# Kernel optimization log

Hardware: AMD Instinct MI355X
Metric: run time of the kernel (lower is better)

The kernel has to match this reference:

```python
import jax, jax.numpy as jnp
import numpy as np

B, NUM_RX, NUM_CHIRPS, SAMPLES = 16, 4, 64, 256
D_BINS, R_BINS = 64, 256


def _conv3d(x, w, b, pad):
    y = jax.lax.conv_general_dilated(x, w, (1, 1, 1), pad,
                                     dimension_numbers=('NCDHW', 'OIDHW', 'NCDHW'))
    return y + b[None, :, None, None, None]


def _conv2d(x, w, b, pad):
    y = jax.lax.conv_general_dilated(x, w, (1, 1), pad,
                                     dimension_numbers=('NCHW', 'OIHW', 'NCHW'))
    return y + b[None, :, None, None]


def _bn2(x, s, t):
    return x * s[None, :, None, None] + t[None, :, None, None]


def _bn3(x, s, t):
    return x * s[None, :, None, None, None] + t[None, :, None, None, None]


def _upsample_bilinear_ac(x, oh, ow):
    # torch Upsample(mode='bilinear', align_corners=True)
    _, _, h, w = x.shape
    ph = jnp.linspace(0.0, h - 1.0, oh)
    pw = jnp.linspace(0.0, w - 1.0, ow)
    h0 = jnp.clip(jnp.floor(ph).astype(jnp.int32), 0, h - 1)
    h1 = jnp.clip(h0 + 1, 0, h - 1)
    fh = ph - h0
    w0 = jnp.clip(jnp.floor(pw).astype(jnp.int32), 0, w - 1)
    w1 = jnp.clip(w0 + 1, 0, w - 1)
    fw = pw - w0
    x = x[:, :, h0, :] * (1.0 - fh)[None, None, :, None] + x[:, :, h1, :] * fh[None, None, :, None]
    x = x[:, :, :, w0] * (1.0 - fw) + x[:, :, :, w1] * fw
    return x


def setup_inputs() -> dict:
    ks = iter(jax.random.split(jax.random.key(0), 80))

    def nrm(shape, s=0.05):
        return s * jax.random.normal(next(ks), shape, dtype=jnp.float32)

    inp = {'x': jax.random.normal(next(ks), (B, NUM_RX, NUM_CHIRPS, SAMPLES, 2), dtype=jnp.float32)}

    def conv(name, shape):
        inp[name + '_w'] = nrm(shape)
        inp[name + '_b'] = nrm((shape[0],))

    def bn(name, n):  # BatchNorm in inference form folded to scale/shift
        inp[name + '_s'] = 1.0 + nrm((n,), 0.1)
        inp[name + '_t'] = nrm((n,), 0.1)

    conv('tc1', (16, 2, 1, 1, 3)); bn('tc1', 16)
    conv('tc2', (32, 16, 1, 1, 3)); bn('tc2', 32)
    conv('rx', (32, 32, NUM_RX, 1, 1)); bn('rx', 32)
    conv('cc1', (64, 32 * NUM_CHIRPS, 3, 3)); bn('cc1', 64)
    conv('cc2', (64, 64, 3, 3)); bn('cc2', 64)
    conv('rd1', (128, 64, 3, 3)); bn('rd1', 128)
    conv('rd2', (128, 128, 3, 3)); bn('rd2', 128)
    conv('up1', (64, 128, 3, 3)); bn('up1', 64)
    conv('up2', (32, 64, 3, 3)); bn('up2', 32)
    conv('up3', (1, 32, 1, 1))
    inp['wr'] = jax.random.normal(next(ks), (SAMPLES, R_BINS, 2), dtype=jnp.float32)
    inp['wd'] = jax.random.normal(next(ks), (NUM_CHIRPS, D_BINS, 2), dtype=jnp.float32)
    return inp


def reference(x, tc1_w, tc1_b, tc1_s, tc1_t, tc2_w, tc2_b, tc2_s, tc2_t,
              rx_w, rx_b, rx_s, rx_t, cc1_w, cc1_b, cc1_s, cc1_t,
              cc2_w, cc2_b, cc2_s, cc2_t, rd1_w, rd1_b, rd1_s, rd1_t,
              rd2_w, rd2_b, rd2_s, rd2_t, up1_w, up1_b, up1_s, up1_t,
              up2_w, up2_b, up2_s, up2_t, up3_w, up3_b, wr, wd):
    r = jax.nn.relu
    p3 = [(0, 0), (0, 0), (1, 1)]
    p2 = [(1, 1), (1, 1)]
    h = jnp.transpose(x, (0, 4, 1, 2, 3))                      # [B,2,RX,C,S]
    h = r(_bn3(_conv3d(h, tc1_w, tc1_b, p3), tc1_s, tc1_t))
    h = r(_bn3(_conv3d(h, tc2_w, tc2_b, p3), tc2_s, tc2_t))
    h = r(_bn3(_conv3d(h, rx_w, rx_b, [(0, 0)] * 3), rx_s, rx_t))[:, :, 0]  # [B,32,C,S]
    h = h.reshape(h.shape[0], -1, SAMPLES)[:, :, None, :]      # [B,32*C,1,S]
    h = r(_bn2(_conv2d(h, cc1_w, cc1_b, p2), cc1_s, cc1_t))
    h = r(_bn2(_conv2d(h, cc2_w, cc2_b, p2), cc2_s, cc2_t))
    h = r(_bn2(_conv2d(h, rd1_w, rd1_b, p2), rd1_s, rd1_t))
    h = r(_bn2(_conv2d(h, rd2_w, rd2_b, p2), rd2_s, rd2_t))
    h = _upsample_bilinear_ac(h, D_BINS, R_BINS)               # [B,128,D,R]
    h = r(_bn2(_conv2d(h, up1_w, up1_b, p2), up1_s, up1_t))
    h = r(_bn2(_conv2d(h, up2_w, up2_b, p2), up2_s, up2_t))
    h = jax.nn.sigmoid(_conv2d(h, up3_w, up3_b, [(0, 0), (0, 0)]))  # [B,1,D,R]
    # learnable_fft (input is real: x_imag = 0), loops -> two batched matmuls
    xr = h[:, 0]                                               # [B,D,R]
    rr = jnp.einsum('bcs,sr->bcr', xr, wr[:, :, 0])            # range DFT, real
    ri = jnp.einsum('bcs,sr->bcr', xr, wr[:, :, 1])            # range DFT, imag
    rdr = jnp.einsum('bcr,cd->bdr', rr, wd[:, :, 0]) - jnp.einsum('bcr,cd->bdr', ri, wd[:, :, 1])
    rdi = jnp.einsum('bcr,cd->bdr', rr, wd[:, :, 1]) + jnp.einsum('bcr,cd->bdr', ri, wd[:, :, 0])
    mag = jnp.sqrt(rdr * rdr + rdi * rdi) / (NUM_CHIRPS * SAMPLES)
    out = jnp.clip(h + 0.1 * mag[:, None], 0.0, 1.0)
    return jnp.transpose(out, (0, 2, 3, 1))                    # [B,D,R,1]
```

## Files before the change

kernel.cpp:

```cpp
#include <hip/hip_runtime.h>
#include <math.h>

#define OFF_A      0u
#define OFF_P      8388608u
#define OFF_WCC1   10485760u
#define OFF_BCC1   10878976u
#define OFF_WCC2   10879040u
#define OFF_BCC2   10895424u
#define OFF_WRD1   10895488u
#define OFF_BRD1   10928256u
#define OFF_WRD2   10928384u
#define OFF_BRD2   10993920u
#define OFF_WUP1   10994048u
#define OFF_BUP1   11092352u
#define OFF_WUP2   11092416u
#define OFF_BUP2   11215296u
#define OFF_WRX    11215328u
#define OFF_W1F    11219424u
#define OFF_B1F    11219520u
#define OFF_W2F    11219536u
#define OFF_B2F    11221072u
#define OFF_BRXF   11221104u
#define OFF_R      0u
#define OFF_H      524288u

__device__ __forceinline__ void fma4(float4& a, const float4& x, float w) {
  a.x = fmaf(x.x, w, a.x); a.y = fmaf(x.y, w, a.y);
  a.z = fmaf(x.z, w, a.z); a.w = fmaf(x.w, w, a.w);
}

__global__ __launch_bounds__(256) void k_repack(
    const float* __restrict__ tc1_w, const float* __restrict__ tc1_b, const float* __restrict__ tc1_s, const float* __restrict__ tc1_t,
    const float* __restrict__ tc2_w, const float* __restrict__ tc2_b, const float* __restrict__ tc2_s, const float* __restrict__ tc2_t,
    const float* __restrict__ rx_w, const float* __restrict__ rx_b, const float* __restrict__ rx_s, const float* __restrict__ rx_t,
    const float* __restrict__ cc1_w, const float* __restrict__ cc1_b, const float* __restrict__ cc1_s, const float* __restrict__ cc1_t,
    const float* __restrict__ cc2_w, const float* __restrict__ cc2_b, const float* __restrict__ cc2_s, const float* __restrict__ cc2_t,
    const float* __restrict__ rd1_w, const float* __restrict__ rd1_b, const float* __restrict__ rd1_s, const float* __restrict__ rd1_t,
    const float* __restrict__ rd2_w, const float* __restrict__ rd2_b, const float* __restrict__ rd2_s, const float* __restrict__ rd2_t,
    const float* __restrict__ up1_w, const float* __restrict__ up1_b, const float* __restrict__ up1_s, const float* __restrict__ up1_t,
    const float* __restrict__ up2_w, const float* __restrict__ up2_b, const float* __restrict__ up2_s, const float* __restrict__ up2_t,
    float* __restrict__ ws)
{
  const int tid = blockIdx.x * blockDim.x + threadIdx.x;
  const int nth = gridDim.x * blockDim.x;

  for (int i = tid; i < 96; i += nth) ws[OFF_W1F + i] = tc1_w[i] * tc1_s[i/6];
  for (int i = tid; i < 16; i += nth) ws[OFF_B1F + i] = tc1_b[i]*tc1_s[i] + tc1_t[i];
  for (int i = tid; i < 1536; i += nth) {
    int oc = i & 31, r = i >> 5, k = r % 3, ic = r / 3;
    ws[OFF_W2F + i] = tc2_w[oc*48 + ic*3 + k] * tc2_s[oc];
  }
  for (int i = tid; i < 32; i += nth) ws[OFF_B2F + i] = tc2_b[i]*tc2_s[i] + tc2_t[i];
  for (int i = tid; i < 4096; i += nth) {
    int oc = i & 31, ic = (i >> 5) & 31, rxi = i >> 10;
    ws[OFF_WRX + i] = rx_w[(oc*32 + ic)*4 + rxi] * rx_s[oc];
  }
  for (int i = tid; i < 32; i += nth) ws[OFF_BRXF + i] = rx_b[i]*rx_s[i] + rx_t[i];

  for (int i = tid; i < 2048*192; i += nth) {
    int c = i / 192, r = i - c*192, k = r >> 6, oc = r & 63;
    ws[OFF_WCC1 + i] = cc1_w[((oc*2048 + c)*3 + 1)*3 + k] * cc1_s[oc];
  }
  for (int i = tid; i < 64; i += nth) ws[OFF_BCC1 + i] = cc1_b[i]*cc1_s[i] + cc1_t[i];

  for (int i = tid; i < 64*64; i += nth) {
    int oc = i & 63, ic = i >> 6;
    float4 v;
    v.x = cc2_w[(oc*64 + ic)*9 + 3] * cc2_s[oc];
    v.y = cc2_w[(oc*64 + ic)*9 + 4] * cc2_s[oc];
    v.z = cc2_w[(oc*64 + ic)*9 + 5] * cc2_s[oc];
    v.w = 0.f;
    ((float4*)(ws + OFF_WCC2))[i] = v;
  }
  for (int i = tid; i < 64; i += nth) ws[OFF_BCC2 + i] = cc2_b[i]*cc2_s[i] + cc2_t[i];

  for (int i = tid; i < 64*128; i += nth) {
    int oc = i & 127, ic = i >> 7;
    float4 v;
    v.x = rd1_w[(oc*64 + ic)*9 + 3] * rd1_s[oc];
    v.y = rd1_w[(oc*64 + ic)*9 + 4] * rd1_s[oc];
    v.z = rd1_w[(oc*64 + ic)*9 + 5] * rd1_s[oc];
    v.w = 0.f;
    ((float4*)(ws + OFF_WRD1))[i] = v;
  }
  for (int i = tid; i < 128; i += nth) ws[OFF_BRD1 + i] = rd1_b[i]*rd1_s[i] + rd1_t[i];

  for (int i = tid; i < 128*128; i += nth) {
    int oc = i & 127, ic = i >> 7;
    float4 v;
    v.x = rd2_w[(oc*128 + ic)*9 + 3] * rd2_s[oc];
    v.y = rd2_w[(oc*128 + ic)*9 + 4] * rd2_s[oc];
    v.z = rd2_w[(oc*128 + ic)*9 + 5] * rd2_s[oc];
    v.w = 0.f;
    ((float4*)(ws + OFF_WRD2))[i] = v;
  }
  for (int i = tid; i < 128; i += nth) ws[OFF_BRD2 + i] = rd2_b[i]*rd2_s[i] + rd2_t[i];

  for (int i = tid; i < 3*128*64; i += nth) {
    int oc = i & 63, ic = (i >> 6) & 127, v = i >> 13;
    const int m = (v == 0) ? 6 : (v == 1) ? 7 : 3;
    float4 o = make_float4(0.f, 0.f, 0.f, 0.f);
    for (int kh = 0; kh < 3; ++kh)
      if ((m >> kh) & 1) {
        o.x += up1_w[((oc*128 + ic)*3 + kh)*3 + 0];
        o.y += up1_w[((oc*128 + ic)*3 + kh)*3 + 1];
        o.z += up1_w[((oc*128 + ic)*3 + kh)*3 + 2];
      }
    o.x *= up1_s[oc]; o.y *= up1_s[oc]; o.z *= up1_s[oc];
    ((float4*)(ws + OFF_WUP1))[i] = o;
  }
  for (int i = tid; i < 64; i += nth) ws[OFF_BUP1 + i] = up1_b[i]*up1_s[i] + up1_t[i];

  for (int i = tid; i < 5*3*64*32; i += nth) {
    int oc = i & 31, ic = (i >> 5) & 63, t = i >> 11;
    int src = t % 3, v = t / 3;
    const int MASKS[15] = {2,4,0,  1,6,0,  0,7,0,  0,3,4,  0,1,2};
    const int m = MASKS[v*3 + src];
    float4 o = make_float4(0.f, 0.f, 0.f, 0.f);
    for (int kh = 0; kh < 3; ++kh)
      if ((m >> kh) & 1) {
        o.x += up2_w[((oc*64 + ic)*3 + kh)*3 + 0];
        o.y += up2_w[((oc*64 + ic)*3 + kh)*3 + 1];
        o.z += up2_w[((oc*64 + ic)*3 + kh)*3 + 2];
      }
    o.x *= up2_s[oc]; o.y *= up2_s[oc]; o.z *= up2_s[oc];
    ((float4*)(ws + OFF_WUP2))[i] = o;
  }
  for (int i = tid; i < 32; i += nth) ws[OFF_BUP2 + i] = up2_b[i]*up2_s[i] + up2_t[i];
}

__global__ __launch_bounds__(128, 4) void k_front(
    const float* __restrict__ x, const float* __restrict__ ws, float* __restrict__ A)
{
  __shared__ float t1s[16][132];
  const int tid = threadIdx.x;
  const int b = blockIdx.x >> 7;
  const int chirp = (blockIdx.x >> 1) & 63;
  const int h = blockIdx.x & 1;
  const int hs0 = h << 7;
  const int s = hs0 + tid;

  const float* w1f  = ws + OFF_W1F;
  const float* b1f  = ws + OFF_B1F;
  const float* w2f  = ws + OFF_W2F;
  const float* b2f  = ws + OFF_B2F;
  const float* wrxf = ws + OFF_WRX;
  const float* brxf = ws + OFF_BRXF;

  float acc[32];
  #pragma unroll
  for (int j = 0; j < 32; ++j) acc[j] = 0.f;

  #pragma unroll 1
  for (int rxi = 0; rxi < 4; ++rxi) {
    const float2* xb2 = (const float2*)(x + ((size_t)(((b*4 + rxi)*64 + chirp)*256) << 1));
    for (int j = tid; j < 130; j += 128) {
      int sc = hs0 - 1 + j;
      if (sc < 0 || sc > 255) {
        #pragma unroll
        for (int o = 0; o < 16; ++o) t1s[o][j] = 0.f;
      } else {
        float2 xm = xb2[sc];
        float2 xl = (sc == 0)   ? make_float2(0.f, 0.f) : xb2[sc-1];
        float2 xr = (sc == 255) ? make_float2(0.f, 0.f) : xb2[sc+1];
        #pragma unroll 4
        for (int o = 0; o < 16; ++o) {
          const float* w = w1f + o*6;
          float v = b1f[o];
          v = fmaf(xl.x, w[0], v);
          v = fmaf(xm.x, w[1], v);
          v = fmaf(xr.x, w[2], v);
          v = fmaf(xl.y, w[3], v);
          v = fmaf(xm.y, w[4], v);
          v = fmaf(xr.y, w[5], v);
          t1s[o][j] = fmaxf(v, 0.f);
        }
      }
    }
    __syncthreads();

    float t2[32];
    #pragma unroll
    for (int j = 0; j < 32; ++j) t2[j] = b2f[j];
    #pragma unroll 2
    for (int ic = 0; ic < 16; ++ic) {
      float tl = t1s[ic][tid];
      float tm = t1s[ic][tid+1];
      float tr = t1s[ic][tid+2];
      const float* w = w2f + ic*96;
      #pragma unroll
      for (int oc = 0; oc < 32; ++oc)
        t2[oc] = fmaf(tl, w[oc], fmaf(tm, w[32+oc], fmaf(tr, w[64+oc], t2[oc])));
    }
    #pragma unroll
    for (int j = 0; j < 32; ++j) t2[j] = fmaxf(t2[j], 0.f);

    const float* wr0 = wrxf + rxi*1024;
    #pragma unroll 4
    for (int ic = 0; ic < 32; ++ic) {
      float tv = t2[ic];
      const float* w = wr0 + ic*32;
      #pragma unroll
      for (int oc = 0; oc < 32; ++oc)
        acc[oc] = fmaf(tv, w[oc], acc[oc]);
    }
    __syncthreads();
  }

  #pragma unroll 4
  for (int oc = 0; oc < 32; ++oc) {
    float v = fmaxf(acc[oc] + brxf[oc], 0.f);
    A[(size_t)((b*2048 + oc*64 + chirp)*256) + s] = v;
  }
}

__global__ __launch_bounds__(128) void k_cc1(
    const float* __restrict__ A, const float* __restrict__ wp, float* __restrict__ P)
{
  __shared__ __align__(16) float As[256][36];
  const int tid = threadIdx.x;
  const int ks = blockIdx.x & 7;
  const int stile = (blockIdx.x >> 3) & 7;
  const int b = blockIdx.x >> 6;
  const int s0 = stile * 32;
  const int ocq = tid & 15;
  const int sg = tid >> 4;
  const int sb = sg * 4;
  const int cbase = ks * 256;

  for (int i = tid; i < 256*36; i += 128) {
    int c = i / 36, si = i - c*36;
    int sA = s0 - 1 + si;
    float v = 0.f;
    if (si < 34 && sA >= 0 && sA < 256)
      v = A[(size_t)(b*2048 + cbase + c)*256 + sA];
    As[c][si] = v;
  }
  __syncthreads();

  float4 acc[4];
  #pragma unroll
  for (int j = 0; j < 4; ++j) acc[j] = make_float4(0.f,0.f,0.f,0.f);

  const float4* w4 = (const float4*)wp;
  #pragma unroll 4
  for (int c = 0; c < 256; ++c) {
    const float4* wc = w4 + (size_t)(cbase + c)*48 + ocq;
    float4 wk0 = wc[0];
    float4 wk1 = wc[16];
    float4 wk2 = wc[32];
    float4 a0 = *(const float4*)&As[c][sb];
    float2 a1 = *(const float2*)&As[c][sb + 4];
    fma4(acc[0], wk0, a0.x); fma4(acc[0], wk1, a0.y); fma4(acc[0], wk2, a0.z);
    fma4(acc[1], wk0, a0.y); fma4(acc[1], wk1, a0.z); fma4(acc[1], wk2, a0.w);
    fma4(acc[2], wk0, a0.z); fma4(acc[2], wk1, a0.w); fma4(acc[2], wk2, a1.x);
    fma4(acc[3], wk0, a0.w); fma4(acc[3], wk1, a1.x); fma4(acc[3], wk2, a1.y);
  }
  float* Pk = P + ((size_t)(ks*16 + b)*256)*64;
  #pragma unroll
  for (int j = 0; j < 4; ++j)
    *(float4*)&Pk[(size_t)(s0 + sb + j)*64 + ocq*4] = acc[j];
}

__global__ __launch_bounds__(256) void k_mid(
    const float* __restrict__ P, const float* __restrict__ bcc1,
    const float* __restrict__ wcc2, const float* __restrict__ bcc2,
    const float* __restrict__ wrd1, const float* __restrict__ brd1,
    const float* __restrict__ wrd2, const float* __restrict__ brd2,
    float* __restrict__ R)
{
  __shared__ __align__(16) float c1s[64][20];
  __shared__ __align__(16) float c2s[64][20];
  __shared__ __align__(16) float r1s[128][12];
  const int tid = threadIdx.x;
  const int b = blockIdx.x >> 5;
  const int s0 = (blockIdx.x & 31) * 8;
  const float4* wc2 = (const float4*)wcc2;
  const float4* wr1 = (const float4*)wrd1;
  const float4* wr2 = (const float4*)wrd2;

  for (int i = tid; i < 64*14; i += 256) {
    int ic = i & 63, si = i >> 6;
    int sA = s0 - 3 + si;
    float v = 0.f;
    if (sA >= 0 && sA < 256) {
      float a = bcc1[ic];
      #pragma unroll
      for (int ksp = 0; ksp < 8; ++ksp)
        a += P[((size_t)(ksp*16 + b)*256 + sA)*64 + ic];
      v = fmaxf(a, 0.f);
    }
    c1s[ic][si] = v;
  }
  __syncthreads();

  {
    const int g = tid >> 6, oc = tid & 63;
    if (g < 3) {
      float bb = bcc2[oc];
      float4 acc = make_float4(bb, bb, bb, bb);
      for (int ic = 0; ic < 64; ++ic) {
        float4 w = wc2[ic*64 + oc];
        float4 ca = *(const float4*)&c1s[ic][g*4];
        float2 cb = *(const float2*)&c1s[ic][g*4 + 4];
        acc.x = fmaf(ca.x,w.x, fmaf(ca.y,w.y, fmaf(ca.z,w.z, acc.x)));
        acc.y = fmaf(ca.y,w.x, fmaf(ca.z,w.y, fmaf(ca.w,w.z, acc.y)));
        acc.z = fmaf(ca.z,w.x, fmaf(ca.w,w.y, fmaf(cb.x,w.z, acc.z)));
        acc.w = fmaf(ca.w,w.x, fmaf(cb.x,w.y, fmaf(cb.y,w.z, acc.w)));
      }
      c2s[oc][g*4+0] = fmaxf(acc.x, 0.f);
      c2s[oc][g*4+1] = fmaxf(acc.y, 0.f);
      c2s[oc][g*4+2] = fmaxf(acc.z, 0.f);
      c2s[oc][g*4+3] = fmaxf(acc.w, 0.f);
    } else {
      int oc2 = tid - 192;
      c2s[oc2][12] = 0.f;
      c2s[oc2][13] = 0.f;
    }
  }
  __syncthreads();

  for (int it = tid; it < 384; it += 256) {
    const int oc = it & 127, g = it >> 7;
    float bb = brd1[oc];
    float4 acc = make_float4(bb, bb, bb, bb);
    for (int ic = 0; ic < 64; ++ic) {
      float4 w = wr1[ic*128 + oc];
      float4 ca = *(const float4*)&c2s[ic][g*4];
      float2 cb = *(const float2*)&c2s[ic][g*4 + 4];
      acc.x = fmaf(ca.x,w.x, fmaf(ca.y,w.y, fmaf(ca.z,w.z, acc.x)));
      acc.y = fmaf(ca.y,w.x, fmaf(ca.z,w.y, fmaf(ca.w,w.z, acc.y)));
      acc.z = fmaf(ca.z,w.x, fmaf(ca.w,w.y, fmaf(cb.x,w.z, acc.z)));
      acc.w = fmaf(ca.w,w.x, fmaf(cb.x,w.y, fmaf(cb.y,w.z, acc.w)));
    }
    if (g*4 + 0 < 12) r1s[oc][g*4+0] = fmaxf(acc.x, 0.f);
    if (g*4 + 1 < 12) r1s[oc][g*4+1] = fmaxf(acc.y, 0.f);
    if (g*4 + 2 < 12) r1s[oc][g*4+2] = fmaxf(acc.z, 0.f);
    if (g*4 + 3 < 12) r1s[oc][g*4+3] = fmaxf(acc.w, 0.f);
  }
  __syncthreads();

  {
    const int g = tid >> 7, oc = tid & 127;
    float bb = brd2[oc];
    float4 acc = make_float4(bb, bb, bb, bb);
    for (int ic = 0; ic < 128; ++ic) {
      float4 w = wr2[ic*128 + oc];
      float4 ca = *(const float4*)&r1s[ic][g*4];
      float2 cb = *(const float2*)&r1s[ic][g*4 + 4];
      acc.x = fmaf(ca.x,w.x, fmaf(ca.y,w.y, fmaf(ca.z,w.z, acc.x)));
      acc.y = fmaf(ca.y,w.x, fmaf(ca.z,w.y, fmaf(ca.w,w.z, acc.y)));
      acc.z = fmaf(ca.z,w.x, fmaf(ca.w,w.y, fmaf(cb.x,w.z, acc.z)));
      acc.w = fmaf(ca.w,w.x, fmaf(cb.x,w.y, fmaf(cb.y,w.z, acc.w)));
    }
    int s = s0 + g*4;
    R[((size_t)b*256 + s+0)*128 + oc] = fmaxf(acc.x, 0.f);
    R[((size_t)b*256 + s+1)*128 + oc] = fmaxf(acc.y, 0.f);
    R[((size_t)b*256 + s+2)*128 + oc] = fmaxf(acc.z, 0.f);
    R[((size_t)b*256 + s+3)*128 + oc] = fmaxf(acc.w, 0.f);
  }
}

__global__ __launch_bounds__(192) void k_up(
    const float* __restrict__ R,
    const float* __restrict__ wup1, const float* __restrict__ bup1,
    const float* __restrict__ wup2, const float* __restrict__ bup2,
    const float* __restrict__ up3_w, const float* __restrict__ up3_b,
    float* __restrict__ H)
{
  __shared__ __align__(16) float Rs[128][12];
  __shared__ __align__(16) float u1s[3][64][12];
  __shared__ float u2s[5][32][9];
  const int tid = threadIdx.x;
  const int b = blockIdx.x >> 5;
  const int s0 = (blockIdx.x & 31) * 8;

  for (int i = tid; i < 128*12; i += 192) {
    int ic = i & 127, si = i >> 7;
    int sA = s0 - 2 + si;
    Rs[ic][si] = (sA >= 0 && sA < 256) ? R[((size_t)b*256 + sA)*128 + ic] : 0.f;
  }
  __syncthreads();

  if (tid < 96) {
    const int vi = tid >> 5, ocp = tid & 31;
    const int oc0 = ocp*2, oc1 = ocp*2 + 1;
    const float4* w4 = (const float4*)wup1;
    float a0[10], a1[10];
    float bb0 = bup1[oc0], bb1 = bup1[oc1];
    #pragma unroll
    for (int p = 0; p < 10; ++p) { a0[p] = bb0; a1[p] = bb1; }
    for (int ic = 0; ic < 128; ++ic) {
      float4 w0 = w4[(vi*128 + ic)*64 + oc0];
      float4 w1 = w4[(vi*128 + ic)*64 + oc1];
      float4 ra = *(const float4*)&Rs[ic][0];
      float4 rb = *(const float4*)&Rs[ic][4];
      float4 rc = *(const float4*)&Rs[ic][8];
      float r[12] = {ra.x,ra.y,ra.z,ra.w, rb.x,rb.y,rb.z,rb.w, rc.x,rc.y,rc.z,rc.w};
      #pragma unroll
      for (int p = 0; p < 10; ++p) {
        a0[p] = fmaf(r[p],w0.x, fmaf(r[p+1],w0.y, fmaf(r[p+2],w0.z, a0[p])));
        a1[p] = fmaf(r[p],w1.x, fmaf(r[p+1],w1.y, fmaf(r[p+2],w1.z, a1[p])));
      }
    }
    #pragma unroll
    for (int p = 0; p < 10; ++p) {
      u1s[vi][oc0][p] = fmaxf(a0[p], 0.f);
      u1s[vi][oc1][p] = fmaxf(a1[p], 0.f);
    }
    u1s[vi][oc0][10] = 0.f; u1s[vi][oc0][11] = 0.f;
    u1s[vi][oc1][10] = 0.f; u1s[vi][oc1][11] = 0.f;
  }
  __syncthreads();

  if (tid < 80) {
    const int v = tid >> 4, ocp = tid & 15;
    const int oc0 = ocp*2, oc1 = ocp*2 + 1;
    const float4* w4 = (const float4*)wup2;
    float a0[8], a1[8];
    float bb0 = bup2[oc0], bb1 = bup2[oc1];
    #pragma unroll
    for (int p = 0; p < 8; ++p) { a0[p] = bb0; a1[p] = bb1; }
    for (int src = 0; src < 3; ++src)
      for (int ic = 0; ic < 64; ++ic) {
        float4 w0 = w4[((v*3 + src)*64 + ic)*32 + oc0];
        float4 w1 = w4[((v*3 + src)*64 + ic)*32 + oc1];
        float4 ua = *(const float4*)&u1s[src][ic][0];
        float4 ub = *(const float4*)&u1s[src][ic][4];
        float2 uc = *(const float2*)&u1s[src][ic][8];
        float r[10] = {ua.x,ua.y,ua.z,ua.w, ub.x,ub.y,ub.z,ub.w, uc.x,uc.y};
        #pragma unroll
        for (int p = 0; p < 8; ++p) {
          a0[p] = fmaf(r[p],w0.x, fmaf(r[p+1],w0.y, fmaf(r[p+2],w0.z, a0[p])));
          a1[p] = fmaf(r[p],w1.x, fmaf(r[p+1],w1.y, fmaf(r[p+2],w1.z, a1[p])));
        }
      }
    #pragma unroll
    for (int p = 0; p < 8; ++p) {
      u2s[v][oc0][p] = fmaxf(a0[p], 0.f);
      u2s[v][oc1][p] = fmaxf(a1[p], 0.f);
    }
  }
  __syncthreads();

  if (tid < 40) {
    int v = tid >> 3, j = tid & 7;
    float a = up3_b[0];
    for (int ic = 0; ic < 32; ++ic)
      a = fmaf(u2s[v][ic][j], up3_w[ic], a);
    H[(size_t)(b*5 + v)*256 + s0 + j] = 1.f / (1.f + expf(-a));
  }
}

__global__ __launch_bounds__(256) void k_spec(
    const float* __restrict__ H, const float* __restrict__ wr, const float* __restrict__ wd,
    float* __restrict__ out)
{
  __shared__ float hs[5][256];
  __shared__ float S0[64], S1[64];
  __shared__ float wds[4][64][2];
  __shared__ float ps[4][64][11];
  const int tid = threadIdx.x;
  const int b = blockIdx.x >> 2;
  const int rt = blockIdx.x & 3;

  for (int i = tid; i < 1280; i += 256) hs[i >> 8][i & 255] = H[(size_t)b*1280 + i];
  if (tid < 64) {
    const float2* wd2 = (const float2*)wd;
    float a0 = 0.f, a1 = 0.f;
    for (int c = 2; c <= 61; ++c) {
      float2 v = wd2[c*64 + tid];
      a0 += v.x; a1 += v.y;
    }
    S0[tid] = a0; S1[tid] = a1;
  }
  for (int i = tid; i < 512; i += 256) {
    int row = i >> 7, rem = i & 127, d = rem >> 1, comp = rem & 1;
    int c = (row < 2) ? row : (60 + row);
    wds[row][d][comp] = wd[(c*64 + d)*2 + comp];
  }
  __syncthreads();

  const int rl = tid & 63;
  const int r = rt*64 + rl;
  const int sq = tid >> 6;
  float rr[5] = {0,0,0,0,0}, ri[5] = {0,0,0,0,0};
  const float2* wr2p = (const float2*)wr;
  for (int s = sq*64; s < sq*64 + 64; ++s) {
    float2 w = wr2p[s*256 + r];
    #pragma unroll
    for (int k = 0; k < 5; ++k) {
      float hv = hs[k][s];
      rr[k] = fmaf(hv, w.x, rr[k]);
      ri[k] = fmaf(hv, w.y, ri[k]);
    }
  }
  #pragma unroll
  for (int k = 0; k < 5; ++k) {
    ps[sq][rl][k]     = rr[k];
    ps[sq][rl][5 + k] = ri[k];
  }
  __syncthreads();

  float Rr[5], Ri[5];
  #pragma unroll
  for (int k = 0; k < 5; ++k) {
    Rr[k] = ps[0][rl][k] + ps[1][rl][k] + ps[2][rl][k] + ps[3][rl][k];
    Ri[k] = ps[0][rl][5+k] + ps[1][rl][5+k] + ps[2][rl][5+k] + ps[3][rl][5+k];
  }
  const int d0 = sq * 16;
  for (int dd = 0; dd < 16; ++dd) {
    int d = d0 + dd;
    float w0r = wds[0][d][0], w0i = wds[0][d][1];
    float w1r = wds[1][d][0], w1i = wds[1][d][1];
    float w2r = wds[2][d][0], w2i = wds[2][d][1];
    float w3r = wds[3][d][0], w3i = wds[3][d][1];
    float s0v = S0[d], s1v = S1[d];
    float rdr = Rr[0]*w0r + Rr[1]*w1r + Rr[2]*s0v + Rr[3]*w2r + Rr[4]*w3r
              - Ri[0]*w0i - Ri[1]*w1i - Ri[2]*s1v - Ri[3]*w2i - Ri[4]*w3i;
    float rdi = Rr[0]*w0i + Rr[1]*w1i + Rr[2]*s1v + Rr[3]*w2i + Rr[4]*w3i
              + Ri[0]*w0r + Ri[1]*w1r + Ri[2]*s0v + Ri[3]*w2r + Ri[4]*w3r;
    float mag = sqrtf(rdr*rdr + rdi*rdi) * (1.0f / 16384.0f);
    int v = (d == 0) ? 0 : (d == 1) ? 1 : (d <= 61) ? 2 : ((d == 62) ? 3 : 4);
    float o = hs[v][r] + 0.1f * mag;
    out[(size_t)b*16384 + d*256 + r] = fminf(fmaxf(o, 0.f), 1.f);
  }
}

extern "C" void kernel_launch(void* const* d_in, const int* in_sizes, int n_in,
                              void* d_out, int out_size, void* d_ws, size_t ws_size,
                              hipStream_t stream)
{
  const float* x     = (const float*)d_in[0];
  const float* tc1_w = (const float*)d_in[1];  const float* tc1_b = (const float*)d_in[2];
  const float* tc1_s = (const float*)d_in[3];  const float* tc1_t = (const float*)d_in[4];
  const float* tc2_w = (const float*)d_in[5];  const float* tc2_b = (const float*)d_in[6];
  const float* tc2_s = (const float*)d_in[7];  const float* tc2_t = (const float*)d_in[8];
  const float* rx_w  = (const float*)d_in[9];  const float* rx_b  = (const float*)d_in[10];
  const float* rx_s  = (const float*)d_in[11]; const float* rx_t  = (const float*)d_in[12];
  const float* cc1_w = (const float*)d_in[13]; const float* cc1_b = (const float*)d_in[14];
  const float* cc1_s = (const float*)d_in[15]; const float* cc1_t = (const float*)d_in[16];
  const float* cc2_w = (const float*)d_in[17]; const float* cc2_b = (const float*)d_in[18];
  const float* cc2_s = (const float*)d_in[19]; const float* cc2_t = (const float*)d_in[20];
  const float* rd1_w = (const float*)d_in[21]; const float* rd1_b = (const float*)d_in[22];
  const float* rd1_s = (const float*)d_in[23]; const float* rd1_t = (const float*)d_in[24];
  const float* rd2_w = (const float*)d_in[25]; const float* rd2_b = (const float*)d_in[26];
  const float* rd2_s = (const float*)d_in[27]; const float* rd2_t = (const float*)d_in[28];
  const float* up1_w = (const float*)d_in[29]; const float* up1_b = (const float*)d_in[30];
  const float* up1_s = (const float*)d_in[31]; const float* up1_t = (const float*)d_in[32];
  const float* up2_w = (const float*)d_in[33]; const float* up2_b = (const float*)d_in[34];
  const float* up2_s = (const float*)d_in[35]; const float* up2_t = (const float*)d_in[36];
  const float* up3_w = (const float*)d_in[37]; const float* up3_b = (const float*)d_in[38];
  const float* wr    = (const float*)d_in[39];
  const float* wd    = (const float*)d_in[40];
  float* ws  = (float*)d_ws;
  float* out = (float*)d_out;

  k_repack<<<1024, 256, 0, stream>>>(tc1_w, tc1_b, tc1_s, tc1_t,
                                     tc2_w, tc2_b, tc2_s, tc2_t,
                                     rx_w, rx_b, rx_s, rx_t,
                                     cc1_w, cc1_b, cc1_s, cc1_t,
                                     cc2_w, cc2_b, cc2_s, cc2_t,
                                     rd1_w, rd1_b, rd1_s, rd1_t,
                                     rd2_w, rd2_b, rd2_s, rd2_t,
                                     up1_w, up1_b, up1_s, up1_t,
                                     up2_w, up2_b, up2_s, up2_t, ws);
  k_front<<<2048, 128, 0, stream>>>(x, ws, ws + OFF_A);
  k_cc1<<<1024, 128, 0, stream>>>(ws + OFF_A, ws + OFF_WCC1, ws + OFF_P);
  k_mid<<<512, 256, 0, stream>>>(ws + OFF_P, ws + OFF_BCC1,
                                 ws + OFF_WCC2, ws + OFF_BCC2,
                                 ws + OFF_WRD1, ws + OFF_BRD1,
                                 ws + OFF_WRD2, ws + OFF_BRD2, ws + OFF_R);
  k_up<<<512, 192, 0, stream>>>(ws + OFF_R, ws + OFF_WUP1, ws + OFF_BUP1,
                                ws + OFF_WUP2, ws + OFF_BUP2, up3_w, up3_b, ws + OFF_H);
  k_spec<<<64, 256, 0, stream>>>(ws + OFF_H, wr, wd, out);
}
```

Baseline: 412.1 us.

## Overlap weight repack with front kernel and widen grids for cc1 and spectral stages

```diff
diff --git a/kernel.cpp b/kernel.cpp
--- a/kernel.cpp
+++ b/kernel.cpp
@@ -29,123 +29,124 @@
   a.z = fmaf(x.z, w, a.z); a.w = fmaf(x.w, w, a.w);
 }
 
-__global__ __launch_bounds__(256) void k_repack(
+__global__ __launch_bounds__(256) void k_repack_front(
     const float* __restrict__ tc1_w, const float* __restrict__ tc1_b, const float* __restrict__ tc1_s, const float* __restrict__ tc1_t,
     const float* __restrict__ tc2_w, const float* __restrict__ tc2_b, const float* __restrict__ tc2_s, const float* __restrict__ tc2_t,
     const float* __restrict__ rx_w, const float* __restrict__ rx_b, const float* __restrict__ rx_s, const float* __restrict__ rx_t,
+    float* __restrict__ ws)
+{
+  const int tid = blockIdx.x * blockDim.x + threadIdx.x;
+  const int nth = gridDim.x * blockDim.x;
+  for (int i = tid; i < 96; i += nth) ws[OFF_W1F + i] = tc1_w[i] * tc1_s[i/6];
+  for (int i = tid; i < 16; i += nth) ws[OFF_B1F + i] = tc1_b[i]*tc1_s[i] + tc1_t[i];
+  for (int i = tid; i < 1536; i += nth) {
+    int oc = i & 31, r = i >> 5, k = r % 3, ic = r / 3;
+    ws[OFF_W2F + i] = tc2_w[oc*48 + ic*3 + k] * tc2_s[oc];
+  }
+  for (int i = tid; i < 32; i += nth) ws[OFF_B2F + i] = tc2_b[i]*tc2_s[i] + tc2_t[i];
+  for (int i = tid; i < 4096; i += nth) {
+    int oc = i & 31, ic = (i >> 5) & 31, rxi = i >> 10;
+    ws[OFF_WRX + i] = rx_w[(oc*32 + ic)*4 + rxi] * rx_s[oc];
+  }
+  for (int i = tid; i < 32; i += nth) ws[OFF_BRXF + i] = rx_b[i]*rx_s[i] + rx_t[i];
+}
+
+__global__ __launch_bounds__(256, 4) void k_front(
+    const float* __restrict__ x, const float* __restrict__ ws_c, float* __restrict__ ws,
     const float* __restrict__ cc1_w, const float* __restrict__ cc1_b, const float* __restrict__ cc1_s, const float* __restrict__ cc1_t,
     const float* __restrict__ cc2_w, const float* __restrict__ cc2_b, const float* __restrict__ cc2_s, const float* __restrict__ cc2_t,
     const float* __restrict__ rd1_w, const float* __restrict__ rd1_b, const float* __restrict__ rd1_s, const float* __restrict__ rd1_t,
     const float* __restrict__ rd2_w, const float* __restrict__ rd2_b, const float* __restrict__ rd2_s, const float* __restrict__ rd2_t,
     const float* __restrict__ up1_w, const float* __restrict__ up1_b, const float* __restrict__ up1_s, const float* __restrict__ up1_t,
     const float* __restrict__ up2_w, const float* __restrict__ up2_b, const float* __restrict__ up2_s, const float* __restrict__ up2_t,
-    float* __restrict__ ws)
-{
-  const int tid = blockIdx.x * blockDim.x + threadIdx.x;
-  const int nth = gridDim.x * blockDim.x;
-
-  for (int i = tid; i < 96; i += nth) ws[OFF_W1F + i] = tc1_w[i] * tc1_s[i/6];
-  for (int i = tid; i < 16; i += nth) ws[OFF_B1F + i] = tc1_b[i]*tc1_s[i] + tc1_t[i];
-  for (int i = tid; i < 1536; i += nth) {
-    int oc = i & 31, r = i >> 5, k = r % 3, ic = r / 3;
-    ws[OFF_W2F + i] = tc2_w[oc*48 + ic*3 + k] * tc2_s[oc];
-  }
-  for (int i = tid; i < 32; i += nth) ws[OFF_B2F + i] = tc2_b[i]*tc2_s[i] + tc2_t[i];
-  for (int i = tid; i < 4096; i += nth) {
-    int oc = i & 31, ic = (i >> 5) & 31, rxi = i >> 10;
-    ws[OFF_WRX + i] = rx_w[(oc*32 + ic)*4 + rxi] * rx_s[oc];
-  }
-  for (int i = tid; i < 32; i += nth) ws[OFF_BRXF + i] = rx_b[i]*rx_s[i] + rx_t[i];
-
-  for (int i = tid; i < 2048*192; i += nth) {
-    int c = i / 192, r = i - c*192, k = r >> 6, oc = r & 63;
-    ws[OFF_WCC1 + i] = cc1_w[((oc*2048 + c)*3 + 1)*3 + k] * cc1_s[oc];
-  }
-  for (int i = tid; i < 64; i += nth) ws[OFF_BCC1 + i] = cc1_b[i]*cc1_s[i] + cc1_t[i];
-
-  for (int i = tid; i < 64*64; i += nth) {
-    int oc = i & 63, ic = i >> 6;
-    float4 v;
-    v.x = cc2_w[(oc*64 + ic)*9 + 3] * cc2_s[oc];
-    v.y = cc2_w[(oc*64 + ic)*9 + 4] * cc2_s[oc];
-    v.z = cc2_w[(oc*64 + ic)*9 + 5] * cc2_s[oc];
-    v.w = 0.f;
-    ((float4*)(ws + OFF_WCC2))[i] = v;
-  }
-  for (int i = tid; i < 64; i += nth) ws[OFF_BCC2 + i] = cc2_b[i]*cc2_s[i] + cc2_t[i];
-
-  for (int i = tid; i < 64*128; i += nth) {
-    int oc = i & 127, ic = i >> 7;
-    float4 v;
-    v.x = rd1_w[(oc*64 + ic)*9 + 3] * rd1_s[oc];
-    v.y = rd1_w[(oc*64 + ic)*9 + 4] * rd1_s[oc];
-    v.z = rd1_w[(oc*64 + ic)*9 + 5] * rd1_s[oc];
-    v.w = 0.f;
-    ((float4*)(ws + OFF_WRD1))[i] = v;
-  }
-  for (int i = tid; i < 128; i += nth) ws[OFF_BRD1 + i] = rd1_b[i]*rd1_s[i] + rd1_t[i];
-
-  for (int i = tid; i < 128*128; i += nth) {
-    int oc = i & 127, ic = i >> 7;
-    float4 v;
-    v.x = rd2_w[(oc*128 + ic)*9 + 3] * rd2_s[oc];
-    v.y = rd2_w[(oc*128 + ic)*9 + 4] * rd2_s[oc];
-    v.z = rd2_w[(oc*128 + ic)*9 + 5] * rd2_s[oc];
-    v.w = 0.f;
-    ((float4*)(ws + OFF_WRD2))[i] = v;
-  }
-  for (int i = tid; i < 128; i += nth) ws[OFF_BRD2 + i] = rd2_b[i]*rd2_s[i] + rd2_t[i];
-
-  for (int i = tid; i < 3*128*64; i += nth) {
-    int oc = i & 63, ic = (i >> 6) & 127, v = i >> 13;
-    const int m = (v == 0) ? 6 : (v == 1) ? 7 : 3;
-    float4 o = make_float4(0.f, 0.f, 0.f, 0.f);
-    for (int kh = 0; kh < 3; ++kh)
-      if ((m >> kh) & 1) {
-        o.x += up1_w[((oc*128 + ic)*3 + kh)*3 + 0];
-        o.y += up1_w[((oc*128 + ic)*3 + kh)*3 + 1];
-        o.z += up1_w[((oc*128 + ic)*3 + kh)*3 + 2];
-      }
-    o.x *= up1_s[oc]; o.y *= up1_s[oc]; o.z *= up1_s[oc];
-    ((float4*)(ws + OFF_WUP1))[i] = o;
-  }
-  for (int i = tid; i < 64; i += nth) ws[OFF_BUP1 + i] = up1_b[i]*up1_s[i] + up1_t[i];
-
-  for (int i = tid; i < 5*3*64*32; i += nth) {
-    int oc = i & 31, ic = (i >> 5) & 63, t = i >> 11;
-    int src = t % 3, v = t / 3;
-    const int MASKS[15] = {2,4,0,  1,6,0,  0,7,0,  0,3,4,  0,1,2};
-    const int m = MASKS[v*3 + src];
-    float4 o = make_float4(0.f, 0.f, 0.f, 0.f);
-    for (int kh = 0; kh < 3; ++kh)
-      if ((m >> kh) & 1) {
-        o.x += up2_w[((oc*64 + ic)*3 + kh)*3 + 0];
-        o.y += up2_w[((oc*64 + ic)*3 + kh)*3 + 1];
-        o.z += up2_w[((oc*64 + ic)*3 + kh)*3 + 2];
-      }
-    o.x *= up2_s[oc]; o.y *= up2_s[oc]; o.z *= up2_s[oc];
-    ((float4*)(ws + OFF_WUP2))[i] = o;
-  }
-  for (int i = tid; i < 32; i += nth) ws[OFF_BUP2 + i] = up2_b[i]*up2_s[i] + up2_t[i];
-}
-
-__global__ __launch_bounds__(128, 4) void k_front(
-    const float* __restrict__ x, const float* __restrict__ ws, float* __restrict__ A)
-{
-  __shared__ float t1s[16][132];
+    float* __restrict__ A)
+{
+  __shared__ float t1s[16][258];
   const int tid = threadIdx.x;
-  const int b = blockIdx.x >> 7;
-  const int chirp = (blockIdx.x >> 1) & 63;
-  const int h = blockIdx.x & 1;
-  const int hs0 = h << 7;
-  const int s = hs0 + tid;
-
-  const float* w1f  = ws + OFF_W1F;
-  const float* b1f  = ws + OFF_B1F;
-  const float* w2f  = ws + OFF_W2F;
-  const float* b2f  = ws + OFF_B2F;
-  const float* wrxf = ws + OFF_WRX;
-  const float* brxf = ws + OFF_BRXF;
+
+  if (blockIdx.x < 64) {
+    const int t = blockIdx.x * 256 + tid;
+    const int nth = 64 * 256;
+    for (int i = t; i < 2048*192; i += nth) {
+      int c = i / 192, r = i - c*192, k = r >> 6, oc = r & 63;
+      ws[OFF_WCC1 + i] = cc1_w[((oc*2048 + c)*3 + 1)*3 + k] * cc1_s[oc];
+    }
+    for (int i = t; i < 64; i += nth) ws[OFF_BCC1 + i] = cc1_b[i]*cc1_s[i] + cc1_t[i];
+    for (int i = t; i < 64*64; i += nth) {
+      int oc = i & 63, ic = i >> 6;
+      float4 v;
+      v.x = cc2_w[(oc*64 + ic)*9 + 3] * cc2_s[oc];
+      v.y = cc2_w[(oc*64 + ic)*9 + 4] * cc2_s[oc];
+      v.z = cc2_w[(oc*64 + ic)*9 + 5] * cc2_s[oc];
+      v.w = 0.f;
+      ((float4*)(ws + OFF_WCC2))[i] = v;
+    }
+    for (int i = t; i < 64; i += nth) ws[OFF_BCC2 + i] = cc2_b[i]*cc2_s[i] + cc2_t[i];
+    for (int i = t; i < 64*128; i += nth) {
+      int oc = i & 127, ic = i >> 7;
+      float4 v;
+      v.x = rd1_w[(oc*64 + ic)*9 + 3] * rd1_s[oc];
+      v.y = rd1_w[(oc*64 + ic)*9 + 4] * rd1_s[oc];
+      v.z = rd1_w[(oc*64 + ic)*9 + 5] * rd1_s[oc];
+      v.w = 0.f;
+      ((float4*)(ws + OFF_WRD1))[i] = v;
+    }
+    for (int i = t; i < 128; i += nth) ws[OFF_BRD1 + i] = rd1_b[i]*rd1_s[i] + rd1_t[i];
+    for (int i = t; i < 128*128; i += nth) {
+      int oc = i & 127, ic = i >> 7;
+      float4 v;
+      v.x = rd2_w[(oc*128 + ic)*9 + 3] * rd2_s[oc];
+      v.y = rd2_w[(oc*128 + ic)*9 + 4] * rd2_s[oc];
+      v.z = rd2_w[(oc*128 + ic)*9 + 5] * rd2_s[oc];
+      v.w = 0.f;
+      ((float4*)(ws + OFF_WRD2))[i] = v;
+    }
+    for (int i = t; i < 128; i += nth) ws[OFF_BRD2 + i] = rd2_b[i]*rd2_s[i] + rd2_t[i];
+    for (int i = t; i < 3*128*64; i += nth) {
+      int oc = i & 63, ic = (i >> 6) & 127, v = i >> 13;
+      const int m = (v == 0) ? 6 : (v == 1) ? 7 : 3;
+      float4 o = make_float4(0.f, 0.f, 0.f, 0.f);
+      for (int kh = 0; kh < 3; ++kh)
+        if ((m >> kh) & 1) {
+          o.x += up1_w[((oc*128 + ic)*3 + kh)*3 + 0];
+          o.y += up1_w[((oc*128 + ic)*3 + kh)*3 + 1];
+          o.z += up1_w[((oc*128 + ic)*3 + kh)*3 + 2];
+        }
+      o.x *= up1_s[oc]; o.y *= up1_s[oc]; o.z *= up1_s[oc];
+      ((float4*)(ws + OFF_WUP1))[i] = o;
+    }
+    for (int i = t; i < 64; i += nth) ws[OFF_BUP1 + i] = up1_b[i]*up1_s[i] + up1_t[i];
+    for (int i = t; i < 5*3*64*32; i += nth) {
+      int oc = i & 31, ic = (i >> 5) & 63, tt = i >> 11;
+      int src = tt % 3, v = tt / 3;
+      const int MASKS[15] = {2,4,0,  1,6,0,  0,7,0,  0,3,4,  0,1,2};
+      const int m = MASKS[v*3 + src];
+      float4 o = make_float4(0.f, 0.f, 0.f, 0.f);
+      for (int kh = 0; kh < 3; ++kh)
+        if ((m >> kh) & 1) {
+          o.x += up2_w[((oc*64 + ic)*3 + kh)*3 + 0];
+          o.y += up2_w[((oc*64 + ic)*3 + kh)*3 + 1];
+          o.z += up2_w[((oc*64 + ic)*3 + kh)*3 + 2];
+        }
+      o.x *= up2_s[oc]; o.y *= up2_s[oc]; o.z *= up2_s[oc];
+      ((float4*)(ws + OFF_WUP2))[i] = o;
+    }
+    for (int i = t; i < 32; i += nth) ws[OFF_BUP2 + i] = up2_b[i]*up2_s[i] + up2_t[i];
+    return;
+  }
+
+  const int bb = blockIdx.x - 64;
+  const int b = bb >> 6, chirp = bb & 63;
+  const int s = tid;
+
+  if (tid < 32) { int o = tid & 15; int c = (tid >> 4) ? 257 : 0; t1s[o][c] = 0.f; }
+
+  const float* w1f  = ws_c + OFF_W1F;
+  const float* b1f  = ws_c + OFF_B1F;
+  const float* w2f  = ws_c + OFF_W2F;
+  const float* b2f  = ws_c + OFF_B2F;
+  const float* wrxf = ws_c + OFF_WRX;
+  const float* brxf = ws_c + OFF_BRXF;
 
   float acc[32];
   #pragma unroll
@@ -153,28 +154,24 @@
 
   #pragma unroll 1
   for (int rxi = 0; rxi < 4; ++rxi) {
-    const float2* xb2 = (const float2*)(x + ((size_t)(((b*4 + rxi)*64 + chirp)*256) << 1));
-    for (int j = tid; j < 130; j += 128) {
-      int sc = hs0 - 1 + j;
-      if (sc < 0 || sc > 255) {
-        #pragma unroll
-        for (int o = 0; o < 16; ++o) t1s[o][j] = 0.f;
-      } else {
-        float2 xm = xb2[sc];
-        float2 xl = (sc == 0)   ? make_float2(0.f, 0.f) : xb2[sc-1];
-        float2 xr = (sc == 255) ? make_float2(0.f, 0.f) : xb2[sc+1];
-        #pragma unroll 4
-        for (int o = 0; o < 16; ++o) {
-          const float* w = w1f + o*6;
-          float v = b1f[o];
-          v = fmaf(xl.x, w[0], v);
-          v = fmaf(xm.x, w[1], v);
-          v = fmaf(xr.x, w[2], v);
-          v = fmaf(xl.y, w[3], v);
-          v = fmaf(xm.y, w[4], v);
-          v = fmaf(xr.y, w[5], v);
-          t1s[o][j] = fmaxf(v, 0.f);
-        }
+    {
+      const float2* xb2 = (const float2*)(x + ((size_t)(((b*4 + rxi)*64 + chirp)*256) << 1));
+      float2 xm = xb2[s];
+      float2 xl = xb2[(s == 0) ? 0 : (s - 1)];
+      float2 xr = xb2[(s == 255) ? 255 : (s + 1)];
+      if (s == 0)   { xl.x = 0.f; xl.y = 0.f; }
+      if (s == 255) { xr.x = 0.f; xr.y = 0.f; }
+      #pragma unroll 4
+      for (int o = 0; o < 16; ++o) {
+        const float* w = w1f + o*6;
+        float v = b1f[o];
+        v = fmaf(xl.x, w[0], v);
+        v = fmaf(xm.x, w[1], v);
+        v = fmaf(xr.x, w[2], v);
+        v = fmaf(xl.y, w[3], v);
+        v = fmaf(xm.y, w[4], v);
+        v = fmaf(xr.y, w[5], v);
+        t1s[o][s+1] = fmaxf(v, 0.f);
       }
     }
     __syncthreads();
@@ -184,9 +181,9 @@
     for (int j = 0; j < 32; ++j) t2[j] = b2f[j];
     #pragma unroll 2
     for (int ic = 0; ic < 16; ++ic) {
-      float tl = t1s[ic][tid];
-      float tm = t1s[ic][tid+1];
-      float tr = t1s[ic][tid+2];
+      float tl = t1s[ic][s];
+      float tm = t1s[ic][s+1];
+      float tr = t1s[ic][s+2];
       const float* w = w2f + ic*96;
       #pragma unroll
       for (int oc = 0; oc < 32; ++oc)
@@ -217,31 +214,29 @@
 __global__ __launch_bounds__(128) void k_cc1(
     const float* __restrict__ A, const float* __restrict__ wp, float* __restrict__ P)
 {
-  __shared__ __align__(16) float As[256][36];
+  __shared__ __align__(16) float As[256][20];
   const int tid = threadIdx.x;
   const int ks = blockIdx.x & 7;
-  const int stile = (blockIdx.x >> 3) & 7;
-  const int b = blockIdx.x >> 6;
-  const int s0 = stile * 32;
+  const int stile = (blockIdx.x >> 3) & 15;
+  const int b = blockIdx.x >> 7;
+  const int s0 = stile * 16;
   const int ocq = tid & 15;
   const int sg = tid >> 4;
-  const int sb = sg * 4;
+  const int sb = sg * 2;
   const int cbase = ks * 256;
 
-  for (int i = tid; i < 256*36; i += 128) {
-    int c = i / 36, si = i - c*36;
+  for (int i = tid; i < 256*20; i += 128) {
+    int c = i / 20, si = i - c*20;
     int sA = s0 - 1 + si;
     float v = 0.f;
-    if (si < 34 && sA >= 0 && sA < 256)
+    if (si < 18 && sA >= 0 && sA < 256)
       v = A[(size_t)(b*2048 + cbase + c)*256 + sA];
     As[c][si] = v;
   }
   __syncthreads();
 
-  float4 acc[4];
-  #pragma unroll
-  for (int j = 0; j < 4; ++j) acc[j] = make_float4(0.f,0.f,0.f,0.f);
-
+  float4 acc0 = make_float4(0.f,0.f,0.f,0.f);
+  float4 acc1 = make_float4(0.f,0.f,0.f,0.f);
   const float4* w4 = (const float4*)wp;
   #pragma unroll 4
   for (int c = 0; c < 256; ++c) {
@@ -249,17 +244,14 @@
     float4 wk0 = wc[0];
     float4 wk1 = wc[16];
     float4 wk2 = wc[32];
-    float4 a0 = *(const float4*)&As[c][sb];
-    float2 a1 = *(const float2*)&As[c][sb + 4];
-    fma4(acc[0], wk0, a0.x); fma4(acc[0], wk1, a0.y); fma4(acc[0], wk2, a0.z);
-    fma4(acc[1], wk0, a0.y); fma4(acc[1], wk1, a0.z); fma4(acc[1], wk2, a0.w);
-    fma4(acc[2], wk0, a0.z); fma4(acc[2], wk1, a0.w); fma4(acc[2], wk2, a1.x);
-    fma4(acc[3], wk0, a0.w); fma4(acc[3], wk1, a1.x); fma4(acc[3], wk2, a1.y);
+    float2 a01 = *(const float2*)&As[c][sb];
+    float2 a23 = *(const float2*)&As[c][sb + 2];
+    fma4(acc0, wk0, a01.x); fma4(acc0, wk1, a01.y); fma4(acc0, wk2, a23.x);
+    fma4(acc1, wk0, a01.y); fma4(acc1, wk1, a23.x); fma4(acc1, wk2, a23.y);
   }
   float* Pk = P + ((size_t)(ks*16 + b)*256)*64;
-  #pragma unroll
-  for (int j = 0; j < 4; ++j)
-    *(float4*)&Pk[(size_t)(s0 + sb + j)*64 + ocq*4] = acc[j];
+  *(float4*)&Pk[(size_t)(s0 + sb + 0)*64 + ocq*4] = acc0;
+  *(float4*)&Pk[(size_t)(s0 + sb + 1)*64 + ocq*4] = acc1;
 }
 
 __global__ __launch_bounds__(256) void k_mid(
@@ -459,10 +451,12 @@
   __shared__ float hs[5][256];
   __shared__ float S0[64], S1[64];
   __shared__ float wds[4][64][2];
-  __shared__ float ps[4][64][11];
+  __shared__ float ps[16][16][10];
+  __shared__ float rred[16][10];
   const int tid = threadIdx.x;
-  const int b = blockIdx.x >> 2;
-  const int rt = blockIdx.x & 3;
+  const int b = blockIdx.x >> 4;
+  const int rt = blockIdx.x & 15;
+  const int r0 = rt * 16;
 
   for (int i = tid; i < 1280; i += 256) hs[i >> 8][i & 255] = H[(size_t)b*1280 + i];
   if (tid < 64) {
@@ -481,49 +475,60 @@
   }
   __syncthreads();
 
-  const int rl = tid & 63;
-  const int r = rt*64 + rl;
-  const int sq = tid >> 6;
-  float rr[5] = {0,0,0,0,0}, ri[5] = {0,0,0,0,0};
-  const float2* wr2p = (const float2*)wr;
-  for (int s = sq*64; s < sq*64 + 64; ++s) {
-    float2 w = wr2p[s*256 + r];
+  {
+    const int rl = tid & 15;
+    const int sq = tid >> 4;
+    const int r = r0 + rl;
+    float rr[5] = {0,0,0,0,0}, ri[5] = {0,0,0,0,0};
+    const float2* wr2p = (const float2*)wr;
+    for (int s = sq*16; s < sq*16 + 16; ++s) {
+      float2 w = wr2p[s*256 + r];
+      #pragma unroll
+      for (int k = 0; k < 5; ++k) {
+        float hv = hs[k][s];
+        rr[k] = fmaf(hv, w.x, rr[k]);
+        ri[k] = fmaf(hv, w.y, ri[k]);
+      }
+    }
     #pragma unroll
     for (int k = 0; k < 5; ++k) {
-      float hv = hs[k][s];
-      rr[k] = fmaf(hv, w.x, rr[k]);
-      ri[k] = fmaf(hv, w.y, ri[k]);
-    }
-  }
-  #pragma unroll
-  for (int k = 0; k < 5; ++k) {
-    ps[sq][rl][k]     = rr[k];
-    ps[sq][rl][5 + k] = ri[k];
-  }
-  __syncthreads();
-
-  float Rr[5], Ri[5];
-  #pragma unroll
-  for (int k = 0; k < 5; ++k) {
-    Rr[k] = ps[0][rl][k] + ps[1][rl][k] + ps[2][rl][k] + ps[3][rl][k];
-    Ri[k] = ps[0][rl][5+k] + ps[1][rl][5+k] + ps[2][rl][5+k] + ps[3][rl][5+k];
-  }
-  const int d0 = sq * 16;
-  for (int dd = 0; dd < 16; ++dd) {
-    int d = d0 + dd;
-    float w0r = wds[0][d][0], w0i = wds[0][d][1];
-    float w1r = wds[1][d][0], w1i = wds[1][d][1];
-    float w2r = wds[2][d][0], w2i = wds[2][d][1];
-    float w3r = wds[3][d][0], w3i = wds[3][d][1];
-    float s0v = S0[d], s1v = S1[d];
-    float rdr = Rr[0]*w0r + Rr[1]*w1r + Rr[2]*s0v + Rr[3]*w2r + Rr[4]*w3r
-              - Ri[0]*w0i - Ri[1]*w1i - Ri[2]*s1v - Ri[3]*w2i - Ri[4]*w3i;
-    float rdi = Rr[0]*w0i + Rr[1]*w1i + Rr[2]*s1v + Rr[3]*w2i + Rr[4]*w3i
-              + Ri[0]*w0r + Ri[1]*w1r + Ri[2]*s0v + Ri[3]*w2r + Ri[4]*w3r;
-    float mag = sqrtf(rdr*rdr + rdi*rdi) * (1.0f / 16384.0f);
-    int v = (d == 0) ? 0 : (d == 1) ? 1 : (d <= 61) ? 2 : ((d == 62) ? 3 : 4);
-    float o = hs[v][r] + 0.1f * mag;
-    out[(size_t)b*16384 + d*256 + r] = fminf(fmaxf(o, 0.f), 1.f);
+      ps[sq][rl][k]     = rr[k];
+      ps[sq][rl][5 + k] = ri[k];
+    }
+  }
+  __syncthreads();
+
+  if (tid < 160) {
+    const int rl = tid & 15, k = tid >> 4;
+    float a = 0.f;
+    #pragma unroll
+    for (int sq = 0; sq < 16; ++sq) a += ps[sq][rl][k];
+    rred[rl][k] = a;
+  }
+  __syncthreads();
+
+  {
+    const int rl = tid & 15, dg = tid >> 4;
+    const int r = r0 + rl;
+    float Rr[5], Ri[5];
+    #pragma unroll
+    for (int k = 0; k < 5; ++k) { Rr[k] = rred[rl][k]; Ri[k] = rred[rl][5 + k]; }
+    for (int dd = 0; dd < 4; ++dd) {
+      int d = dg*4 + dd;
+      float w0r = wds[0][d][0], w0i = wds[0][d][1];
+      float w1r = wds[1][d][0], w1i = wds[1][d][1];
+      float w2r = wds[2][d][0], w2i = wds[2][d][1];
+      float w3r = wds[3][d][0], w3i = wds[3][d][1];
+      float s0v = S0[d], s1v = S1[d];
+      float rdr = Rr[0]*w0r + Rr[1]*w1r + Rr[2]*s0v + Rr[3]*w2r + Rr[4]*w3r
+                - Ri[0]*w0i - Ri[1]*w1i - Ri[2]*s1v - Ri[3]*w2i - Ri[4]*w3i;
+      float rdi = Rr[0]*w0i + Rr[1]*w1i + Rr[2]*s1v + Rr[3]*w2i + Rr[4]*w3i
+                + Ri[0]*w0r + Ri[1]*w1r + Ri[2]*s0v + Ri[3]*w2r + Ri[4]*w3r;
+      float mag = sqrtf(rdr*rdr + rdi*rdi) * (1.0f / 16384.0f);
+      int v = (d == 0) ? 0 : (d == 1) ? 1 : (d <= 61) ? 2 : ((d == 62) ? 3 : 4);
+      float o = hs[v][r] + 0.1f * mag;
+      out[(size_t)b*16384 + d*256 + r] = fminf(fmaxf(o, 0.f), 1.f);
+    }
   }
 }
 
@@ -556,22 +561,23 @@
   float* ws  = (float*)d_ws;
   float* out = (float*)d_out;
 
-  k_repack<<<1024, 256, 0, stream>>>(tc1_w, tc1_b, tc1_s, tc1_t,
-                                     tc2_w, tc2_b, tc2_s, tc2_t,
-                                     rx_w, rx_b, rx_s, rx_t,
-                                     cc1_w, cc1_b, cc1_s, cc1_t,
-                                     cc2_w, cc2_b, cc2_s, cc2_t,
-                                     rd1_w, rd1_b, rd1_s, rd1_t,
-                                     rd2_w, rd2_b, rd2_s, rd2_t,
-                                     up1_w, up1_b, up1_s, up1_t,
-                                     up2_w, up2_b, up2_s, up2_t, ws);
-  k_front<<<2048, 128, 0, stream>>>(x, ws, ws + OFF_A);
-  k_cc1<<<1024, 128, 0, stream>>>(ws + OFF_A, ws + OFF_WCC1, ws + OFF_P);
+  k_repack_front<<<8, 256, 0, stream>>>(tc1_w, tc1_b, tc1_s, tc1_t,
+                                        tc2_w, tc2_b, tc2_s, tc2_t,
+                                        rx_w, rx_b, rx_s, rx_t, ws);
+  k_front<<<1088, 256, 0, stream>>>(x, ws, ws,
+                                    cc1_w, cc1_b, cc1_s, cc1_t,
+                                    cc2_w, cc2_b, cc2_s, cc2_t,
+                                    rd1_w, rd1_b, rd1_s, rd1_t,
+                                    rd2_w, rd2_b, rd2_s, rd2_t,
+                                    up1_w, up1_b, up1_s, up1_t,
+                                    up2_w, up2_b, up2_s, up2_t,
+                                    ws + OFF_A);
+  k_cc1<<<2048, 128, 0, stream>>>(ws + OFF_A, ws + OFF_WCC1, ws + OFF_P);
   k_mid<<<512, 256, 0, stream>>>(ws + OFF_P, ws + OFF_BCC1,
                                  ws + OFF_WCC2, ws + OFF_BCC2,
                                  ws + OFF_WRD1, ws + OFF_BRD1,
                                  ws + OFF_WRD2, ws + OFF_BRD2, ws + OFF_R);
   k_up<<<512, 192, 0, stream>>>(ws + OFF_R, ws + OFF_WUP1, ws + OFF_BUP1,
                                 ws + OFF_WUP2, ws + OFF_BUP2, up3_w, up3_b, ws + OFF_H);
-  k_spec<<<64, 256, 0, stream>>>(ws + OFF_H, wr, wd, out);
-}
+  k_spec<<<256, 256, 0, stream>>>(ws + OFF_H, wr, wd, out);
+}
```

New measurement: 415.4 us. Within noise of the previous version (+0.8%).
